# Kernel optimization log

Measured on AMD Instinct MI355X. Metric: run time of the kernel, lower is better.

The kernel has to match this reference:

```python
import jax, jax.numpy as jnp
import numpy as np

N_NODES = 50000
N_EDGES = 800000
IN_DIM = 128
OUT_DIM = 128
NUM_HEADS = 8
HEAD_DIM = OUT_DIM // NUM_HEADS
LN_EPS = 1e-5


def setup_inputs() -> dict:
    key = jax.random.key(0)
    ks = jax.random.split(key, 8)
    # xavier-uniform bounds
    def xavier(k, shape, fan_in, fan_out):
        a = float(np.sqrt(6.0 / (fan_in + fan_out)))
        return jax.random.uniform(k, shape, jnp.float32, -a, a)
    x = jax.random.normal(ks[0], (N_NODES, IN_DIM), jnp.float32)
    edge_index = jax.random.randint(ks[1], (2, N_EDGES), 0, N_NODES, jnp.int32)
    # store Linear weights as (in, out) so forward is x @ W (same math as torch x @ W.T)
    W_src = xavier(ks[2], (IN_DIM, OUT_DIM), IN_DIM, OUT_DIM)
    W_dst = xavier(ks[3], (IN_DIM, OUT_DIM), IN_DIM, OUT_DIM)
    attn = xavier(ks[4], (NUM_HEADS, HEAD_DIM), HEAD_DIM, NUM_HEADS)
    W_out = xavier(ks[5], (OUT_DIM, OUT_DIM), OUT_DIM, OUT_DIM)
    b_out = jnp.zeros((OUT_DIM,), jnp.float32)
    gamma = jnp.ones((OUT_DIM,), jnp.float32)
    beta = jnp.zeros((OUT_DIM,), jnp.float32)
    return {"x": x, "edge_index": edge_index, "W_src": W_src, "W_dst": W_dst,
            "attn": attn, "W_out": W_out, "b_out": b_out, "gamma": gamma, "beta": beta}


def reference(x, edge_index, W_src, W_dst, attn, W_out, b_out, gamma, beta):
    N = x.shape[0]
    H, D = attn.shape
    src, dst = edge_index[0], edge_index[1]
    # node transforms: (N, H, D)
    h_src = (x @ W_src).reshape(N, H, D)
    h_dst = (x @ W_dst).reshape(N, H, D)
    # per-edge GATv2 attention logits (E, H)
    h_src_e = h_src[src]                                  # (E, H, D)
    e = jax.nn.leaky_relu(h_src_e + h_dst[dst], 0.2)
    s = jnp.einsum('ehd,hd->eh', e, attn)
    # segment (scatter) softmax over incoming edges of each dst node
    m = jax.ops.segment_max(s, dst, num_segments=N)       # (N, H)
    exp = jnp.exp(s - m[dst])
    denom = jax.ops.segment_sum(exp, dst, num_segments=N)
    alpha = exp / (denom[dst] + 1e-8)                     # (E, H)
    # weighted message aggregation
    msg = (h_src_e * alpha[..., None]).reshape(-1, H * D)
    out = jax.ops.segment_sum(msg, dst, num_segments=N)   # (N, H*D)
    out = out @ W_out + b_out
    out = out + x                                          # residual (in_dim == out_dim)
    # LayerNorm
    mu = jnp.mean(out, axis=-1, keepdims=True)
    var = jnp.var(out, axis=-1, keepdims=True)
    out = (out - mu) * jax.lax.rsqrt(var + LN_EPS) * gamma + beta
    return out
```

## Files before the change

kernel.cpp:

```cpp
#include <hip/hip_runtime.h>
#include <hip/hip_bf16.h>

#define HEADS 8
#define CDIM 128
#define CAP 96
#define CHUNK 2048
#define LOG2E 1.44269504088896f

typedef __attribute__((ext_vector_type(8))) short bf16x8;
typedef __attribute__((ext_vector_type(4))) float f32x4;
typedef __attribute__((ext_vector_type(2))) _Float16 h16x2;

__device__ __forceinline__ unsigned short f2bs(float f) {
    union { __hip_bfloat16 b; unsigned short u; } c;
    c.b = __float2bfloat16(f);
    return c.u;
}

__device__ __forceinline__ unsigned short f2hs(float f) {
    union { _Float16 h; unsigned short u; } c;
    c.h = (_Float16)f;
    return c.u;
}

__global__ __launch_bounds__(256) void init_kernel(
        int* __restrict__ cnt,
        const float* __restrict__ Wsrc,
        const float* __restrict__ Wdst,
        const float* __restrict__ Wout,
        unsigned short* __restrict__ WT,
        unsigned short* __restrict__ WoT, int N, int nzblk) {
    const int b = blockIdx.x;
    if (b < nzblk) {
        const int i = b * 256 + threadIdx.x;
        if (i < N) cnt[i] = 0;
        return;
    }
    const int i = (b - nzblk) * 256 + threadIdx.x;
    if (i < 16384)      { WT[i] = f2bs(Wsrc[(i & 127) * CDIM + (i >> 7)]); }
    else if (i < 32768) { int j = i - 16384; WT[16384 + j] = f2bs(Wdst[(j & 127) * CDIM + (j >> 7)]); }
    else if (i < 49152) { int j = i - 32768; WoT[j] = f2bs(Wout[(j & 127) * CDIM + (j >> 7)]); }
}

__global__ __launch_bounds__(256) void fused_bucket_transform(
        const int* __restrict__ ei,
        int* __restrict__ cnt,
        int* __restrict__ bucket,
        const float* __restrict__ x,
        const unsigned short* __restrict__ WT,
        unsigned short* __restrict__ hsrc,
        unsigned short* __restrict__ hdst,
        int N, int E, int ngemm, int nbucket) {
    const int g = blockIdx.x;
    const bool is_gemm = ((g % 5) == 4) && ((g / 5) < ngemm);
    if (!is_gemm) {
        const int bid = g - g / 5;
        if (bid >= nbucket) return;
        const int shard = bid & 7;
        const int base = (bid >> 3) * CHUNK;
        int end = base + CHUNK; if (end > E) end = E;
        for (int e = base + (int)threadIdx.x; e < end; e += 256) {
            const int dst = ei[E + e];
            if ((dst & 7) == shard) {
                const int src = ei[e];
                const int pos = atomicAdd(&cnt[dst], 1);
                if (pos < CAP) bucket[(size_t)dst * CAP + pos] = src;
            }
        }
        return;
    }
    __shared__ unsigned short As[64][136];
    __shared__ unsigned short Bs[128][136];
    const int t = threadIdx.x;
    const int m0 = (g / 5) * 64;
    for (int i = t; i < 64 * 32; i += 256) {
        const int r = i >> 5, kq = i & 31;
        const int gr = m0 + r;
        float4 v = make_float4(0.f, 0.f, 0.f, 0.f);
        if (gr < N) v = *(const float4*)(x + (size_t)gr * CDIM + kq * 4);
        uint2 pk;
        pk.x = (unsigned)f2bs(v.x) | ((unsigned)f2bs(v.y) << 16);
        pk.y = (unsigned)f2bs(v.z) | ((unsigned)f2bs(v.w) << 16);
        *(uint2*)&As[r][kq * 4] = pk;
    }
    const int w = t >> 6, lane = t & 63, l16 = lane & 15, quad = lane >> 4;
    const int wm = (w & 1) * 32, wn = (w >> 1) * 64;
#pragma unroll
    for (int half = 0; half < 2; half++) {
        const unsigned short* Wb = WT + (size_t)half * 16384;
        for (int i = t; i < 128 * 16; i += 256) {
            const int r = i >> 4, q = i & 15;
            *(uint4*)&Bs[r][q * 8] = *(const uint4*)(Wb + (size_t)r * CDIM + q * 8);
        }
        __syncthreads();
        f32x4 acc[2][4];
#pragma unroll
        for (int mi = 0; mi < 2; mi++)
#pragma unroll
            for (int ni = 0; ni < 4; ni++) acc[mi][ni] = (f32x4){0.f, 0.f, 0.f, 0.f};
#pragma unroll
        for (int kc = 0; kc < 4; kc++) {
            const int k0 = kc * 32 + quad * 8;
            bf16x8 af[2], bf[4];
            af[0] = *(const bf16x8*)&As[wm + l16][k0];
            af[1] = *(const bf16x8*)&As[wm + 16 + l16][k0];
#pragma unroll
            for (int ni = 0; ni < 4; ni++)
                bf[ni] = *(const bf16x8*)&Bs[wn + ni * 16 + l16][k0];
#pragma unroll
            for (int mi = 0; mi < 2; mi++)
#pragma unroll
                for (int ni = 0; ni < 4; ni++)
                    acc[mi][ni] = __builtin_amdgcn_mfma_f32_16x16x32_bf16(af[mi], bf[ni], acc[mi][ni], 0, 0, 0);
        }
        unsigned short* H = half ? hdst : hsrc;
#pragma unroll
        for (int mi = 0; mi < 2; mi++)
#pragma unroll
            for (int reg = 0; reg < 4; reg++) {
                const int gm = m0 + wm + mi * 16 + quad * 4 + reg;
                if (gm < N) {
#pragma unroll
                    for (int ni = 0; ni < 4; ni++)
                        H[(size_t)gm * CDIM + wn + ni * 16 + l16] = f2hs(acc[mi][ni][reg]);
                }
            }
        __syncthreads();
    }
}

__global__ __launch_bounds__(256) void attn_agg6(
        const unsigned short* __restrict__ hsrc,
        const unsigned short* __restrict__ hdst,
        const float* __restrict__ attn,
        const int* __restrict__ cnt,
        const int* __restrict__ bucket,
        unsigned short* __restrict__ aggb) {
    __shared__ int src_lds[4][CAP];
    const int t = threadIdx.x;
    const int w = t >> 6, lane = t & 63;
    const int dst = blockIdx.x * 4 + w;
    int deg = cnt[dst];
    deg = deg > CAP ? CAP : deg;
    for (int j = lane; j < deg; j += 64)
        src_lds[w][j] = bucket[(size_t)dst * CAP + j];

    const int l32 = lane & 31;
    const int eh = lane >> 5;
    const uint2 hdu = *(const uint2*)(hdst + (size_t)dst * CDIM + l32 * 4);
    const h16x2 hd01 = __builtin_bit_cast(h16x2, hdu.x);
    const h16x2 hd23 = __builtin_bit_cast(h16x2, hdu.y);
    const float4 a4 = ((const float4*)attn)[l32];
    h16x2 a01, a23;
    a01[0] = (_Float16)(a4.x * LOG2E); a01[1] = (_Float16)(a4.y * LOG2E);
    a23[0] = (_Float16)(a4.z * LOG2E); a23[1] = (_Float16)(a4.w * LOG2E);
    const h16x2 k02 = { (_Float16)0.2f, (_Float16)0.2f };

    const unsigned short* hb = hsrc + l32 * 4;

    float l = 0.f, acc0 = 0.f, acc1 = 0.f, acc2 = 0.f, acc3 = 0.f;
    for (int j0 = 0; j0 < deg; j0 += 8) {
        uint2 vv[4];
#pragma unroll
        for (int p = 0; p < 4; p++) {
            const int j = j0 + 2 * p + eh;
            const int sj = (j < deg) ? src_lds[w][j] : 0;
            vv[p] = *(const uint2*)(hb + (size_t)sj * CDIM);
        }
#pragma unroll
        for (int p = 0; p < 4; p++) {
            const int j = j0 + 2 * p + eh;
            const h16x2 v01 = __builtin_bit_cast(h16x2, vv[p].x);
            const h16x2 v23 = __builtin_bit_cast(h16x2, vv[p].y);
            h16x2 e01 = v01 + hd01;
            h16x2 e23 = v23 + hd23;
            e01 = __builtin_elementwise_max(e01, e01 * k02);
            e23 = __builtin_elementwise_max(e23, e23 * k02);
            float pp = __builtin_amdgcn_fdot2(e01, a01, 0.f, false);
            pp = __builtin_amdgcn_fdot2(e23, a23, pp, false);
            pp += __int_as_float(__builtin_amdgcn_update_dpp(0, __float_as_int(pp), 0xB1, 0xF, 0xF, true));
            pp += __int_as_float(__builtin_amdgcn_update_dpp(0, __float_as_int(pp), 0x4E, 0xF, 0xF, true));
            float wgt = __builtin_amdgcn_exp2f(pp);
            wgt = (j < deg) ? wgt : 0.f;
            l += wgt;
            acc0 = fmaf(wgt, (float)v01[0], acc0);
            acc1 = fmaf(wgt, (float)v01[1], acc1);
            acc2 = fmaf(wgt, (float)v23[0], acc2);
            acc3 = fmaf(wgt, (float)v23[1], acc3);
        }
    }
    l    += __shfl_xor(l, 32);
    acc0 += __shfl_xor(acc0, 32);
    acc1 += __shfl_xor(acc1, 32);
    acc2 += __shfl_xor(acc2, 32);
    acc3 += __shfl_xor(acc3, 32);
    if (lane < 32) {
        const float r = 1.f / (l + 1e-8f);
        uint2 o;
        o.x = (unsigned)f2bs(acc0 * r) | ((unsigned)f2bs(acc1 * r) << 16);
        o.y = (unsigned)f2bs(acc2 * r) | ((unsigned)f2bs(acc3 * r) << 16);
        *(uint2*)(aggb + (size_t)dst * CDIM + l32 * 4) = o;
    }
}

__global__ __launch_bounds__(256) void out_mfma_ln64(
        const unsigned short* __restrict__ aggb,
        const float* __restrict__ x,
        const unsigned short* __restrict__ WoT,
        const float* __restrict__ bo,
        const float* __restrict__ gam,
        const float* __restrict__ bet,
        float* __restrict__ out, int N) {
    __shared__ unsigned short As[64][136];
    __shared__ unsigned short Bs[128][136];
    __shared__ float red1[64][2], red2[64][2];
    __shared__ float s_mu[64], s_rs[64];
    const int t = threadIdx.x;
    const int m0 = blockIdx.x * 64;
    for (int i = t; i < 64 * 16; i += 256) {
        const int r = i >> 4, q = i & 15;
        const int gr = m0 + r;
        uint4 v = make_uint4(0u, 0u, 0u, 0u);
        if (gr < N) v = *(const uint4*)(aggb + (size_t)gr * CDIM + q * 8);
        *(uint4*)&As[r][q * 8] = v;
    }
    for (int i = t; i < 128 * 16; i += 256) {
        const int r = i >> 4, q = i & 15;
        *(uint4*)&Bs[r][q * 8] = *(const uint4*)(WoT + (size_t)r * CDIM + q * 8);
    }
    __syncthreads();
    const int w = t >> 6, lane = t & 63, l16 = lane & 15, quad = lane >> 4;
    const int wm = (w & 1) * 32, wn = (w >> 1) * 64;
    f32x4 acc[2][4];
#pragma unroll
    for (int mi = 0; mi < 2; mi++)
#pragma unroll
        for (int ni = 0; ni < 4; ni++) acc[mi][ni] = (f32x4){0.f, 0.f, 0.f, 0.f};
#pragma unroll
    for (int kc = 0; kc < 4; kc++) {
        const int k0 = kc * 32 + quad * 8;
        bf16x8 af[2], bf[4];
        af[0] = *(const bf16x8*)&As[l16 + wm][k0];
        af[1] = *(const bf16x8*)&As[l16 + wm + 16][k0];
#pragma unroll
        for (int ni = 0; ni < 4; ni++)
            bf[ni] = *(const bf16x8*)&Bs[wn + ni * 16 + l16][k0];
#pragma unroll
        for (int mi = 0; mi < 2; mi++)
#pragma unroll
            for (int ni = 0; ni < 4; ni++)
                acc[mi][ni] = __builtin_amdgcn_mfma_f32_16x16x32_bf16(af[mi], bf[ni], acc[mi][ni], 0, 0, 0);
    }
    float bi[4], g4[4], be4[4];
#pragma unroll
    for (int ni = 0; ni < 4; ni++) {
        const int n = wn + ni * 16 + l16;
        bi[ni] = bo[n]; g4[ni] = gam[n]; be4[ni] = bet[n];
    }
#pragma unroll
    for (int mi = 0; mi < 2; mi++)
#pragma unroll
        for (int reg = 0; reg < 4; reg++) {
            const int gm = m0 + wm + mi * 16 + quad * 4 + reg;
#pragma unroll
            for (int ni = 0; ni < 4; ni++) {
                const float xr = (gm < N) ? x[(size_t)gm * CDIM + wn + ni * 16 + l16] : 0.f;
                acc[mi][ni][reg] += bi[ni] + xr;
            }
        }
#pragma unroll
    for (int mi = 0; mi < 2; mi++)
#pragma unroll
        for (int reg = 0; reg < 4; reg++) {
            float s1 = acc[mi][0][reg] + acc[mi][1][reg] + acc[mi][2][reg] + acc[mi][3][reg];
            float s2 = acc[mi][0][reg] * acc[mi][0][reg] + acc[mi][1][reg] * acc[mi][1][reg]
                     + acc[mi][2][reg] * acc[mi][2][reg] + acc[mi][3][reg] * acc[mi][3][reg];
            s1 += __shfl_xor(s1, 1, 16); s1 += __shfl_xor(s1, 2, 16);
            s1 += __shfl_xor(s1, 4, 16); s1 += __shfl_xor(s1, 8, 16);
            s2 += __shfl_xor(s2, 1, 16); s2 += __shfl_xor(s2, 2, 16);
            s2 += __shfl_xor(s2, 4, 16); s2 += __shfl_xor(s2, 8, 16);
            if (l16 == 0) {
                const int row = wm + mi * 16 + quad * 4 + reg;
                red1[row][w >> 1] = s1;
                red2[row][w >> 1] = s2;
            }
        }
    __syncthreads();
    if (t < 64) {
        const float s1 = red1[t][0] + red1[t][1];
        const float s2 = red2[t][0] + red2[t][1];
        const float mu = s1 * (1.f / 128.f);
        const float var = s2 * (1.f / 128.f) - mu * mu;
        s_mu[t] = mu;
        s_rs[t] = rsqrtf(var + 1e-5f);
    }
    __syncthreads();
#pragma unroll
    for (int mi = 0; mi < 2; mi++)
#pragma unroll
        for (int reg = 0; reg < 4; reg++) {
            const int row = wm + mi * 16 + quad * 4 + reg;
            const int gm = m0 + row;
            if (gm < N) {
                const float mu = s_mu[row], rs = s_rs[row];
#pragma unroll
                for (int ni = 0; ni < 4; ni++)
                    out[(size_t)gm * CDIM + wn + ni * 16 + l16] =
                        (acc[mi][ni][reg] - mu) * rs * g4[ni] + be4[ni];
            }
        }
}

extern "C" void kernel_launch(void* const* d_in, const int* in_sizes, int n_in,
                              void* d_out, int out_size, void* d_ws, size_t ws_size,
                              hipStream_t stream) {
    const float* x    = (const float*)d_in[0];
    const int*   ei   = (const int*)d_in[1];
    const float* Wsrc = (const float*)d_in[2];
    const float* Wdst = (const float*)d_in[3];
    const float* attn = (const float*)d_in[4];
    const float* Wout = (const float*)d_in[5];
    const float* bo   = (const float*)d_in[6];
    const float* gam  = (const float*)d_in[7];
    const float* bet  = (const float*)d_in[8];
    float* out = (float*)d_out;

    const int N = in_sizes[0] / CDIM;
    const int E = in_sizes[1] / 2;
    const int NX = N * CDIM;

    unsigned short* hsrc_h = (unsigned short*)d_ws;
    unsigned short* hdst_h = hsrc_h + (size_t)NX;
    unsigned short* aggb   = hdst_h + (size_t)NX;
    unsigned short* WT     = aggb + (size_t)NX;
    unsigned short* WoT    = WT + 32768;
    int* cnt    = (int*)(WoT + 16384);
    int* bucket = cnt + N;

    const int nzblk    = (N + 255) / 256;
    const int nwblk    = 49152 / 256;
    const int ngroups  = (E + CHUNK - 1) / CHUNK;
    const int nbucket  = ngroups * 8;
    const int ngemm    = (N + 63) / 64;

    init_kernel<<<nzblk + nwblk, 256, 0, stream>>>(cnt, Wsrc, Wdst, Wout, WT, WoT, N, nzblk);
    fused_bucket_transform<<<nbucket + ngemm, 256, 0, stream>>>(
        ei, cnt, bucket, x, WT, hsrc_h, hdst_h, N, E, ngemm, nbucket);
    attn_agg6<<<N / 4, 256, 0, stream>>>(hsrc_h, hdst_h, attn, cnt, bucket, aggb);
    out_mfma_ln64<<<(N + 63) / 64, 256, 0, stream>>>(aggb, x, WoT, bo, gam, bet, out, N);
}
```

Measured before the change: 201.6 us.

## Split fused bucket/GEMM kernel into separate launches and batch edge loads

Separates the interleaved bucketing and node-transform GEMM blocks of the single fused kernel into two kernels, giving up the overlap of atomic-heavy bucketing with MFMA work. The bucket kernel now loads all 8 edges per thread up front (unrolled) before doing the atomics, exposing more memory-level parallelism. The cost is an extra launch and no concurrency between the two phases. The GEMM block no longer pays for the shared-memory footprint when it only runs bucketing.

```diff
diff --git a/kernel.cpp b/kernel.cpp
--- a/kernel.cpp
+++ b/kernel.cpp
@@ -42,37 +42,40 @@
     else if (i < 49152) { int j = i - 32768; WoT[j] = f2bs(Wout[(j & 127) * CDIM + (j >> 7)]); }
 }
 
-__global__ __launch_bounds__(256) void fused_bucket_transform(
+__global__ __launch_bounds__(256) void bucket_kernel(
         const int* __restrict__ ei,
         int* __restrict__ cnt,
-        int* __restrict__ bucket,
+        int* __restrict__ bucket, int E) {
+    const int bid = blockIdx.x;
+    const int shard = bid & 7;
+    const int base = (bid >> 3) * CHUNK + (int)threadIdx.x;
+    int d[8], s[8];
+#pragma unroll
+    for (int q = 0; q < 8; q++) {
+        const int idx = base + q * 256;
+        const int safe = idx < E ? idx : 0;
+        d[q] = ei[E + safe];
+        s[q] = ei[safe];
+    }
+#pragma unroll
+    for (int q = 0; q < 8; q++) {
+        const int idx = base + q * 256;
+        if (idx < E && (d[q] & 7) == shard) {
+            const int pos = atomicAdd(&cnt[d[q]], 1);
+            if (pos < CAP) bucket[(size_t)d[q] * CAP + pos] = s[q];
+        }
+    }
+}
+
+__global__ __launch_bounds__(256) void transform_mfma64f(
         const float* __restrict__ x,
         const unsigned short* __restrict__ WT,
         unsigned short* __restrict__ hsrc,
-        unsigned short* __restrict__ hdst,
-        int N, int E, int ngemm, int nbucket) {
-    const int g = blockIdx.x;
-    const bool is_gemm = ((g % 5) == 4) && ((g / 5) < ngemm);
-    if (!is_gemm) {
-        const int bid = g - g / 5;
-        if (bid >= nbucket) return;
-        const int shard = bid & 7;
-        const int base = (bid >> 3) * CHUNK;
-        int end = base + CHUNK; if (end > E) end = E;
-        for (int e = base + (int)threadIdx.x; e < end; e += 256) {
-            const int dst = ei[E + e];
-            if ((dst & 7) == shard) {
-                const int src = ei[e];
-                const int pos = atomicAdd(&cnt[dst], 1);
-                if (pos < CAP) bucket[(size_t)dst * CAP + pos] = src;
-            }
-        }
-        return;
-    }
+        unsigned short* __restrict__ hdst, int N) {
     __shared__ unsigned short As[64][136];
     __shared__ unsigned short Bs[128][136];
     const int t = threadIdx.x;
-    const int m0 = (g / 5) * 64;
+    const int m0 = blockIdx.x * 64;
     for (int i = t; i < 64 * 32; i += 256) {
         const int r = i >> 5, kq = i & 31;
         const int gr = m0 + r;
@@ -341,11 +344,10 @@
     const int nwblk    = 49152 / 256;
     const int ngroups  = (E + CHUNK - 1) / CHUNK;
     const int nbucket  = ngroups * 8;
-    const int ngemm    = (N + 63) / 64;
 
     init_kernel<<<nzblk + nwblk, 256, 0, stream>>>(cnt, Wsrc, Wdst, Wout, WT, WoT, N, nzblk);
-    fused_bucket_transform<<<nbucket + ngemm, 256, 0, stream>>>(
-        ei, cnt, bucket, x, WT, hsrc_h, hdst_h, N, E, ngemm, nbucket);
+    bucket_kernel<<<nbucket, 256, 0, stream>>>(ei, cnt, bucket, E);
+    transform_mfma64f<<<(N + 63) / 64, 256, 0, stream>>>(x, WT, hsrc_h, hdst_h, N);
     attn_agg6<<<N / 4, 256, 0, stream>>>(hsrc_h, hdst_h, attn, cnt, bucket, aggb);
     out_mfma_ln64<<<(N + 63) / 64, 256, 0, stream>>>(aggb, x, WoT, bo, gam, bet, out, N);
 }
```

After: 200.4 us. No clear change (-0.6%).
